# Performance work log

Hardware: AMD Instinct MI355X
Metric: run time of the kernel (lower is better)

## Reference

```python
import jax, jax.numpy as jnp
import numpy as np

H = 16      # attention_head_num
DH = 64     # attention_head_size
D = H * DH  # out_dim = 1024


def setup_inputs() -> dict:
    key = jax.random.key(0)
    ks = jax.random.split(key, 9)
    s = 1.0 / np.sqrt(D)
    x = jax.random.normal(ks[0], (2, 2048, D), dtype=jnp.float32)
    Wq = jax.random.uniform(ks[1], (D, D), jnp.float32, -s, s)
    bq = jax.random.uniform(ks[2], (D,), jnp.float32, -s, s)
    Wk = jax.random.uniform(ks[3], (D, D), jnp.float32, -s, s)
    bk = jax.random.uniform(ks[4], (D,), jnp.float32, -s, s)
    Wv = jax.random.uniform(ks[5], (D, D), jnp.float32, -s, s)
    bv = jax.random.uniform(ks[6], (D,), jnp.float32, -s, s)
    Wo = jax.random.uniform(ks[7], (D, D), jnp.float32, -s, s)
    bo = jax.random.uniform(ks[8], (D,), jnp.float32, -s, s)
    return {"x": x, "Wq": Wq, "bq": bq, "Wk": Wk, "bk": bk,
            "Wv": Wv, "bv": bv, "Wo": Wo, "bo": bo}


def reference(x, Wq, bq, Wk, bk, Wv, bv, Wo, bo):
    B, S, _ = x.shape
    # projections (nn.Linear: x @ W^T + b)
    q = (x @ Wq.T + bq).reshape(B, S, H, DH).transpose(0, 2, 1, 3)  # [B,H,S,Dh]
    k = (x @ Wk.T + bk).reshape(B, S, H, DH).transpose(0, 2, 1, 3)
    v = (x @ Wv.T + bv).reshape(B, S, H, DH).transpose(0, 2, 1, 3)
    scores = jnp.einsum('bhqd,bhkd->bhqk', q, k) / jnp.sqrt(jnp.float32(DH))
    probs = jax.nn.softmax(scores, axis=-1)  # dropout is identity in eval mode
    ctx = jnp.einsum('bhqk,bhkd->bhqd', probs, v)
    ctx = ctx.transpose(0, 2, 1, 3).reshape(B, S, D)
    return ctx @ Wo.T + bo
```

## Files before the change

### kernel.cpp

```cpp
#include <hip/hip_runtime.h>
#include <hip/hip_bf16.h>
#include <stdint.h>

typedef __attribute__((ext_vector_type(8))) short bf16x8;
typedef __attribute__((ext_vector_type(8))) unsigned short u16x8;
typedef __attribute__((ext_vector_type(4))) unsigned short u16x4;
typedef __attribute__((ext_vector_type(4))) float f32x4;

constexpr int NB  = 2;
constexpr int NS  = 2048;
constexpr int NH  = 16;
constexpr int NDH = 64;
constexpr int ND  = 1024;

static __device__ __forceinline__ unsigned short bfbits(float f) {
    union { float f; uint32_t u; } v; v.f = f;
    uint32_t u = v.u + 0x7FFFu + ((v.u >> 16) & 1u);
    return (unsigned short)(u >> 16);
}

static __device__ __forceinline__ float fexp2(float x) {
#if __has_builtin(__builtin_amdgcn_exp2f)
    return __builtin_amdgcn_exp2f(x);
#else
    return exp2f(x);
#endif
}

static __device__ __forceinline__ void gl_lds16(const void* g, void* l) {
    __builtin_amdgcn_global_load_lds(
        (const __attribute__((address_space(1))) unsigned int*)g,
        (__attribute__((address_space(3))) unsigned int*)l, 16, 0, 0);
}

__global__ __launch_bounds__(256)
void cvt_kernel(const float* __restrict__ x,  const float* __restrict__ wq,
                const float* __restrict__ wk, const float* __restrict__ wv,
                const float* __restrict__ wo,
                unsigned short* __restrict__ xb,  unsigned short* __restrict__ wqb,
                unsigned short* __restrict__ wkb, unsigned short* __restrict__ wvb,
                unsigned short* __restrict__ wob)
{
    const int b = blockIdx.x;
    const float* s; unsigned short* d; int off;
    if      (b < 2048) { s = x;  d = xb;  off = b; }
    else if (b < 2560) { s = wq; d = wqb; off = b - 2048; }
    else if (b < 3072) { s = wk; d = wkb; off = b - 2560; }
    else if (b < 3584) { s = wv; d = wvb; off = b - 3072; }
    else               { s = wo; d = wob; off = b - 3584; }
    const size_t idx = ((size_t)off * 256 + threadIdx.x) * 8;
    float4 f0 = *(const float4*)&s[idx];
    float4 f1 = *(const float4*)&s[idx + 4];
    u16x8 o;
    o[0] = bfbits(f0.x); o[1] = bfbits(f0.y); o[2] = bfbits(f0.z); o[3] = bfbits(f0.w);
    o[4] = bfbits(f1.x); o[5] = bfbits(f1.y); o[6] = bfbits(f1.z); o[7] = bfbits(f1.w);
    *(u16x8*)&d[idx] = o;
}

__global__ __launch_bounds__(256, 2)
void qkv_kernel(const unsigned short* __restrict__ xb,
                const unsigned short* __restrict__ wqb,
                const unsigned short* __restrict__ wkb,
                const unsigned short* __restrict__ wvb,
                const float* __restrict__ bq, const float* __restrict__ bk,
                const float* __restrict__ bv,
                unsigned short* __restrict__ qbuf,
                unsigned short* __restrict__ kbuf,
                unsigned short* __restrict__ vtbuf)
{
    __shared__ unsigned short As[128 * 64];
    __shared__ unsigned short Bs[128 * 64];
    __shared__ unsigned short Tt[128][136];

    const int fid = blockIdx.x + blockIdx.y * 24;
    const int xcd = fid & 7, idx = fid >> 3;
    const int bx  = idx >> 2;
    const int by  = xcd * 4 + (idx & 3);

    const int m0  = by * 128;
    const int jg0 = bx * 128;
    const int proj = jg0 >> 10;
    const int n0   = jg0 & 1023;
    const unsigned short* W = (proj == 0) ? wqb : (proj == 1) ? wkb : wvb;
    const float* bias       = (proj == 0) ? bq  : (proj == 1) ? bk  : bv;

    const int tid = threadIdx.x, lane = tid & 63, wid = tid >> 6;
    const int wm = wid >> 1, wn = wid & 1;
    const int l15 = lane & 15, g = lane >> 4;

    const f32x4 fzero = {0.f, 0.f, 0.f, 0.f};
    f32x4 acc[4][4];
#pragma unroll
    for (int i = 0; i < 4; i++)
#pragma unroll
        for (int j = 0; j < 4; j++) acc[i][j] = fzero;

    const int srow = tid >> 3;
    const int scb  = ((tid & 7) * 16) ^ ((srow & 7) << 4);
    const char* asrc = (const char*)xb + (size_t)(m0 + srow) * 2048 + scb;
    const char* bsrc = (const char*)W  + (size_t)(n0 + srow) * 2048 + scb;
    char* adst = (char*)As + tid * 16;
    char* bdst = (char*)Bs + tid * 16;
    const int xm = (l15 & 7) << 4;

    for (int k0 = 0; k0 < 1024; k0 += 64) {
#pragma unroll
        for (int i = 0; i < 4; i++) {
            gl_lds16(asrc + (size_t)i * 32 * 2048 + k0 * 2, adst + i * 4096);
            gl_lds16(bsrc + (size_t)i * 32 * 2048 + k0 * 2, bdst + i * 4096);
        }
        __syncthreads();
#pragma unroll
        for (int kk = 0; kk < 2; kk++) {
            bf16x8 af[4], bfr[4];
#pragma unroll
            for (int i = 0; i < 4; i++) {
                const int row = wm * 64 + i * 16 + l15;
                af[i] = *(const bf16x8*)((const char*)As + row * 128 + ((kk * 64 + g * 16) ^ xm));
            }
#pragma unroll
            for (int j = 0; j < 4; j++) {
                const int row = wn * 64 + j * 16 + l15;
                bfr[j] = *(const bf16x8*)((const char*)Bs + row * 128 + ((kk * 64 + g * 16) ^ xm));
            }
#pragma unroll
            for (int i = 0; i < 4; i++)
#pragma unroll
                for (int j = 0; j < 4; j++)
                    acc[i][j] = __builtin_amdgcn_mfma_f32_16x16x32_bf16(af[i], bfr[j], acc[i][j], 0, 0, 0);
        }
        __syncthreads();
    }

    if (proj < 2) {
        unsigned short* qk_out = (proj == 0) ? qbuf : kbuf;
        const float qs = (proj == 0) ? 0.18033688f : 1.0f;
#pragma unroll
        for (int j = 0; j < 4; j++) {
            const int col = n0 + wn * 64 + j * 16 + l15;
            const float bsv = bias[col];
            const int h = col >> 6, dh = col & 63;
#pragma unroll
            for (int i = 0; i < 4; i++)
#pragma unroll
                for (int r = 0; r < 4; r++) {
                    const int row = m0 + wm * 64 + i * 16 + g * 4 + r;
                    const int b_ = row >> 11, s_ = row & (NS - 1);
                    qk_out[((size_t)((b_ * NH + h) * NS + s_)) * NDH + dh] =
                        bfbits((acc[i][j][r] + bsv) * qs);
                }
        }
    } else {
#pragma unroll
        for (int j = 0; j < 4; j++) {
            const int cl = wn * 64 + j * 16 + l15;
            const float bsv = bias[n0 + cl];
#pragma unroll
            for (int i = 0; i < 4; i++) {
                u16x4 w4;
#pragma unroll
                for (int r = 0; r < 4; r++) w4[r] = bfbits(acc[i][j][r] + bsv);
                *(u16x4*)&Tt[cl][wm * 64 + i * 16 + g * 4] = w4;
            }
        }
        __syncthreads();
        const int b_ = m0 >> 11, s0 = m0 & (NS - 1);
        const int h0 = n0 >> 6;
#pragma unroll
        for (int it = 0; it < 8; it++) {
            const int c = wid * 32 + it * 4 + g;
            u16x8 v8 = *(const u16x8*)&Tt[c][l15 * 8];
            const size_t row = (size_t)(b_ * NH + h0 + (c >> 6)) * NDH + (c & 63);
            *(u16x8*)&vtbuf[row * NS + s0 + l15 * 8] = v8;
        }
    }
}

__global__ __launch_bounds__(512, 4)
void attn_kernel(const unsigned short* __restrict__ qbuf,
                 const unsigned short* __restrict__ kbuf,
                 const unsigned short* __restrict__ vtbuf,
                 unsigned short* __restrict__ ctxbuf)
{
    __shared__ unsigned short Ks[4][64 * 64];
    __shared__ unsigned short Vs[4][64 * 64];

    const int fid  = blockIdx.x + blockIdx.y * 16;
    const int nid  = (fid % 8) * 64 + fid / 8;
    const int bx   = nid % 16, bh = nid / 16;
    const int q0   = bx * 128;

    const int tid = threadIdx.x, lane = tid & 63, wid = tid >> 6;
    const int l15 = lane & 15, g = lane >> 4;

    const unsigned short* qb = qbuf  + (size_t)bh * NS * NDH;
    const unsigned short* kb = kbuf  + (size_t)bh * NS * NDH;
    const unsigned short* vb = vtbuf + (size_t)bh * NDH * NS;

    const int qrow = q0 + wid * 16 + l15;
    const bf16x8 qf0 = *(const bf16x8*)&qb[(size_t)qrow * NDH + g * 8];
    const bf16x8 qf1 = *(const bf16x8*)&qb[(size_t)qrow * NDH + 32 + g * 8];

    const short oneb = (short)0x3F80;
    const bf16x8 ones = {oneb, oneb, oneb, oneb, oneb, oneb, oneb, oneb};

    const f32x4 fzero = {0.f, 0.f, 0.f, 0.f};
    f32x4 acc[4];
#pragma unroll
    for (int d = 0; d < 4; d++) acc[d] = fzero;
    f32x4 acc_l = fzero;

    const int o = tid * 16;
    const int srow = o >> 7;
    const int scb  = (o & 127) ^ ((srow & 7) << 4);
    const char* ksrc = (const char*)kb + srow * 128 + scb;
    const char* vsrc = (const char*)vb + (size_t)srow * (NS * 2) + scb;
    char* kbase = (char*)Ks;
    char* vbase = (char*)Vs;
    const int xm = (l15 & 7) << 4;

    auto STAGE = [&](int b, int t_) {
        gl_lds16(ksrc + (size_t)t_ * 8192, kbase + b * 8192 + o);
        gl_lds16(vsrc + (size_t)t_ * 128,  vbase + b * 8192 + o);
    };

    auto QK = [&](int h, f32x4 (&sv)[4]) {
        const char* ksb = kbase + (h & 3) * 8192;
        __builtin_amdgcn_s_setprio(1);
#pragma unroll
        for (int kt = 0; kt < 4; kt++) {
            const char* rb = ksb + (kt * 16 + l15) * 128;
            bf16x8 kf0 = *(const bf16x8*)(rb + ((g * 16) ^ xm));
            bf16x8 kf1 = *(const bf16x8*)(rb + ((64 + g * 16) ^ xm));
            f32x4 s4 = fzero;
            s4 = __builtin_amdgcn_mfma_f32_16x16x32_bf16(kf0, qf0, s4, 0, 0, 0);
            s4 = __builtin_amdgcn_mfma_f32_16x16x32_bf16(kf1, qf1, s4, 0, 0, 0);
            sv[kt] = s4;
        }
        __builtin_amdgcn_s_setprio(0);
    };

    auto SMPV = [&](int h, f32x4 (&sv)[4]) {
        const char* vsb = vbase + (h & 3) * 8192;
#pragma unroll
        for (int kt = 0; kt < 4; kt++)
#pragma unroll
            for (int r = 0; r < 4; r++)
                sv[kt][r] = fexp2(sv[kt][r]);

        bf16x8 pf[2];
#pragma unroll
        for (int f = 0; f < 2; f++) {
            const int kt0 = f * 2;
            union { __hip_bfloat162 h2; uint32_t u; } c0, c1, c2, c3;
            float2 p01 = { sv[kt0][0], sv[kt0][1] };
            float2 p23 = { sv[kt0][2], sv[kt0][3] };
            float2 p45 = { sv[kt0 + 1][0], sv[kt0 + 1][1] };
            float2 p67 = { sv[kt0 + 1][2], sv[kt0 + 1][3] };
            c0.h2 = __float22bfloat162_rn(p01);
            c1.h2 = __float22bfloat162_rn(p23);
            c2.h2 = __float22bfloat162_rn(p45);
            c3.h2 = __float22bfloat162_rn(p67);
            uint32_t a0 = c0.u, a1 = c1.u, b0 = c2.u, b1 = c3.u;
            asm("v_permlane32_swap_b32 %0, %1" : "+v"(a0), "+v"(b0));
            asm("v_permlane32_swap_b32 %0, %1" : "+v"(a1), "+v"(b1));
            asm("v_permlane16_swap_b32 %0, %1" : "+v"(a0), "+v"(b0));
            asm("v_permlane16_swap_b32 %0, %1" : "+v"(a1), "+v"(b1));
            union { uint32_t w[4]; bf16x8 fr; } r_;
            r_.w[0] = a0; r_.w[1] = a1; r_.w[2] = b0; r_.w[3] = b1;
            pf[f] = r_.fr;
        }

        __builtin_amdgcn_s_setprio(1);
        acc_l = __builtin_amdgcn_mfma_f32_16x16x32_bf16(pf[0], ones, acc_l, 0, 0, 0);
        acc_l = __builtin_amdgcn_mfma_f32_16x16x32_bf16(pf[1], ones, acc_l, 0, 0, 0);
#pragma unroll
        for (int d = 0; d < 4; d++) {
            const char* rb = vsb + (d * 16 + l15) * 128;
            bf16x8 vf0 = *(const bf16x8*)(rb + ((g * 16) ^ xm));
            bf16x8 vf1 = *(const bf16x8*)(rb + ((64 + g * 16) ^ xm));
            acc[d] = __builtin_amdgcn_mfma_f32_16x16x32_bf16(pf[0], vf0, acc[d], 0, 0, 0);
            acc[d] = __builtin_amdgcn_mfma_f32_16x16x32_bf16(pf[1], vf1, acc[d], 0, 0, 0);
        }
        __builtin_amdgcn_s_setprio(0);
    };

    f32x4 svA[4], svB[4];

    STAGE(0, 0); STAGE(1, 1); STAGE(2, 2);
    asm volatile("s_waitcnt vmcnt(4)" ::: "memory");
    __builtin_amdgcn_s_barrier();
    asm volatile("" ::: "memory");
    QK(0, svA);

    for (int t = 0; t < 30; t += 2) {
        asm volatile("s_waitcnt vmcnt(2)" ::: "memory");
        __builtin_amdgcn_s_barrier();
        asm volatile("" ::: "memory");
        STAGE((t + 3) & 3, t + 3);
        QK(t + 1, svB);
        SMPV(t, svA);

        asm volatile("s_waitcnt vmcnt(2)" ::: "memory");
        __builtin_amdgcn_s_barrier();
        asm volatile("" ::: "memory");
        if (t + 4 < 32) STAGE((t + 4) & 3, t + 4);
        QK(t + 2, svA);
        SMPV(t + 1, svB);
    }
    asm volatile("s_waitcnt vmcnt(0)" ::: "memory");
    __builtin_amdgcn_s_barrier();
    asm volatile("" ::: "memory");
    QK(31, svB);
    SMPV(30, svA);
    SMPV(31, svB);

    const int b_ = bh >> 4, h_ = bh & 15;
#pragma unroll
    for (int r = 0; r < 4; r++) {
        const float inv = 1.f / acc_l[r];
        const int sq = q0 + wid * 16 + g * 4 + r;
        const size_t base = ((size_t)(b_ * NS + sq)) * ND + h_ * NDH;
#pragma unroll
        for (int d = 0; d < 4; d++)
            ctxbuf[base + d * 16 + l15] = bfbits(acc[d][r] * inv);
    }
}

__global__ __launch_bounds__(256, 2)
void out_kernel(const unsigned short* __restrict__ ctx,
                const unsigned short* __restrict__ wob,
                const float* __restrict__ bo,
                float* __restrict__ out)
{
    __shared__ unsigned short As[128 * 64];
    __shared__ unsigned short Bs[128 * 64];

    const int n0 = blockIdx.x * 128;
    const int m0 = blockIdx.y * 128;
    const int tid = threadIdx.x, lane = tid & 63, wid = tid >> 6;
    const int wm = wid >> 1, wn = wid & 1;
    const int l15 = lane & 15, g = lane >> 4;

    const f32x4 fzero = {0.f, 0.f, 0.f, 0.f};
    f32x4 acc[4][4];
#pragma unroll
    for (int i = 0; i < 4; i++)
#pragma unroll
        for (int j = 0; j < 4; j++) acc[i][j] = fzero;

    const int srow = tid >> 3;
    const int scb  = ((tid & 7) * 16) ^ ((srow & 7) << 4);
    const char* asrc = (const char*)ctx + (size_t)(m0 + srow) * 2048 + scb;
    const char* bsrc = (const char*)wob + (size_t)(n0 + srow) * 2048 + scb;
    char* adst = (char*)As + tid * 16;
    char* bdst = (char*)Bs + tid * 16;
    const int xm = (l15 & 7) << 4;

    for (int k0 = 0; k0 < 1024; k0 += 64) {
#pragma unroll
        for (int i = 0; i < 4; i++) {
            gl_lds16(asrc + (size_t)i * 32 * 2048 + k0 * 2, adst + i * 4096);
            gl_lds16(bsrc + (size_t)i * 32 * 2048 + k0 * 2, bdst + i * 4096);
        }
        __syncthreads();
#pragma unroll
        for (int kk = 0; kk < 2; kk++) {
            bf16x8 af[4], bfr[4];
#pragma unroll
            for (int i = 0; i < 4; i++) {
                const int row = wm * 64 + i * 16 + l15;
                af[i] = *(const bf16x8*)((const char*)As + row * 128 + ((kk * 64 + g * 16) ^ xm));
            }
#pragma unroll
            for (int j = 0; j < 4; j++) {
                const int row = wn * 64 + j * 16 + l15;
                bfr[j] = *(const bf16x8*)((const char*)Bs + row * 128 + ((kk * 64 + g * 16) ^ xm));
            }
#pragma unroll
            for (int i = 0; i < 4; i++)
#pragma unroll
                for (int j = 0; j < 4; j++)
                    acc[i][j] = __builtin_amdgcn_mfma_f32_16x16x32_bf16(af[i], bfr[j], acc[i][j], 0, 0, 0);
        }
        __syncthreads();
    }

#pragma unroll
    for (int j = 0; j < 4; j++) {
        const int col = n0 + wn * 64 + j * 16 + l15;
        const float bsv = bo[col];
#pragma unroll
        for (int i = 0; i < 4; i++)
#pragma unroll
            for (int r = 0; r < 4; r++) {
                const int row = m0 + wm * 64 + i * 16 + g * 4 + r;
                out[(size_t)row * ND + col] = acc[i][j][r] + bsv;
            }
    }
}

extern "C" void kernel_launch(void* const* d_in, const int* in_sizes, int n_in,
                              void* d_out, int out_size, void* d_ws, size_t ws_size,
                              hipStream_t stream) {
    const float* x  = (const float*)d_in[0];
    const float* Wq = (const float*)d_in[1];
    const float* bq = (const float*)d_in[2];
    const float* Wk = (const float*)d_in[3];
    const float* bk = (const float*)d_in[4];
    const float* Wv = (const float*)d_in[5];
    const float* bv = (const float*)d_in[6];
    const float* Wo = (const float*)d_in[7];
    const float* bo = (const float*)d_in[8];
    float* out = (float*)d_out;

    const size_t qk_elems = (size_t)NB * NH * NS * NDH;
    const size_t w_elems  = (size_t)ND * ND;
    unsigned short* qbuf   = (unsigned short*)d_ws;
    unsigned short* kbuf   = qbuf + qk_elems;
    unsigned short* vtbuf  = kbuf + qk_elems;
    unsigned short* ctxbuf = vtbuf + qk_elems;
    unsigned short* xb     = ctxbuf + qk_elems;
    unsigned short* wqb    = xb + qk_elems;
    unsigned short* wkb    = wqb + w_elems;
    unsigned short* wvb    = wkb + w_elems;
    unsigned short* wob    = wvb + w_elems;

    cvt_kernel<<<4096, 256, 0, stream>>>(x, Wq, Wk, Wv, Wo, xb, wqb, wkb, wvb, wob);
    qkv_kernel<<<dim3(24, 32), 256, 0, stream>>>(xb, wqb, wkb, wvb, bq, bk, bv,
                                                 qbuf, kbuf, vtbuf);
    attn_kernel<<<dim3(16, 32), 512, 0, stream>>>(qbuf, kbuf, vtbuf, ctxbuf);
    out_kernel<<<dim3(8, 32), 256, 0, stream>>>(ctxbuf, wob, bo, out);
}
```

Measured before the change: 115.6 us.

## Process two 16-row query tiles per wave in attention kernel

Each attention wave now handles 32 query rows (two 16-row sub-tiles) instead of 16, so a block covers 256 queries and the grid halves to 8x32 blocks. K and V fragments read from LDS are reused across both sub-tiles, halving global K/V staging traffic and LDS reads per query. The cost is roughly doubled accumulator and score registers, with launch bounds relaxed from 4 to 2 blocks per CU, which lowers occupancy and latency hiding. There are also only 256 blocks, which may underfill the GPU's CUs.

```diff
diff --git a/kernel.cpp b/kernel.cpp
--- a/kernel.cpp
+++ b/kernel.cpp
@@ -176,7 +176,7 @@
     }
 }
 
-__global__ __launch_bounds__(512, 4)
+__global__ __launch_bounds__(512, 2)
 void attn_kernel(const unsigned short* __restrict__ qbuf,
                  const unsigned short* __restrict__ kbuf,
                  const unsigned short* __restrict__ vtbuf,
@@ -185,10 +185,10 @@
     __shared__ unsigned short Ks[4][64 * 64];
     __shared__ unsigned short Vs[4][64 * 64];
 
-    const int fid  = blockIdx.x + blockIdx.y * 16;
-    const int nid  = (fid % 8) * 64 + fid / 8;
-    const int bx   = nid % 16, bh = nid / 16;
-    const int q0   = bx * 128;
+    const int fid  = blockIdx.x + blockIdx.y * 8;
+    const int nid  = (fid & 7) * 32 + (fid >> 3);
+    const int bx   = nid & 7, bh = nid >> 3;
+    const int q0   = bx * 256;
 
     const int tid = threadIdx.x, lane = tid & 63, wid = tid >> 6;
     const int l15 = lane & 15, g = lane >> 4;
@@ -197,18 +197,24 @@
     const unsigned short* kb = kbuf  + (size_t)bh * NS * NDH;
     const unsigned short* vb = vtbuf + (size_t)bh * NDH * NS;
 
-    const int qrow = q0 + wid * 16 + l15;
-    const bf16x8 qf0 = *(const bf16x8*)&qb[(size_t)qrow * NDH + g * 8];
-    const bf16x8 qf1 = *(const bf16x8*)&qb[(size_t)qrow * NDH + 32 + g * 8];
+    bf16x8 qf[2][2];
+#pragma unroll
+    for (int u = 0; u < 2; u++) {
+        const int qrow = q0 + wid * 32 + u * 16 + l15;
+        qf[u][0] = *(const bf16x8*)&qb[(size_t)qrow * NDH + g * 8];
+        qf[u][1] = *(const bf16x8*)&qb[(size_t)qrow * NDH + 32 + g * 8];
+    }
 
     const short oneb = (short)0x3F80;
     const bf16x8 ones = {oneb, oneb, oneb, oneb, oneb, oneb, oneb, oneb};
 
     const f32x4 fzero = {0.f, 0.f, 0.f, 0.f};
-    f32x4 acc[4];
-#pragma unroll
-    for (int d = 0; d < 4; d++) acc[d] = fzero;
-    f32x4 acc_l = fzero;
+    f32x4 acc[2][4];
+#pragma unroll
+    for (int u = 0; u < 2; u++)
+#pragma unroll
+        for (int d = 0; d < 4; d++) acc[u][d] = fzero;
+    f32x4 acc_l[2] = {fzero, fzero};
 
     const int o = tid * 16;
     const int srow = o >> 7;
@@ -224,7 +230,7 @@
         gl_lds16(vsrc + (size_t)t_ * 128,  vbase + b * 8192 + o);
     };
 
-    auto QK = [&](int h, f32x4 (&sv)[4]) {
+    auto QK = [&](int h, f32x4 (&sv)[2][4]) {
         const char* ksb = kbase + (h & 3) * 8192;
         __builtin_amdgcn_s_setprio(1);
 #pragma unroll
@@ -232,60 +238,73 @@
             const char* rb = ksb + (kt * 16 + l15) * 128;
             bf16x8 kf0 = *(const bf16x8*)(rb + ((g * 16) ^ xm));
             bf16x8 kf1 = *(const bf16x8*)(rb + ((64 + g * 16) ^ xm));
-            f32x4 s4 = fzero;
-            s4 = __builtin_amdgcn_mfma_f32_16x16x32_bf16(kf0, qf0, s4, 0, 0, 0);
-            s4 = __builtin_amdgcn_mfma_f32_16x16x32_bf16(kf1, qf1, s4, 0, 0, 0);
-            sv[kt] = s4;
+#pragma unroll
+            for (int u = 0; u < 2; u++) {
+                f32x4 s4 = fzero;
+                s4 = __builtin_amdgcn_mfma_f32_16x16x32_bf16(kf0, qf[u][0], s4, 0, 0, 0);
+                s4 = __builtin_amdgcn_mfma_f32_16x16x32_bf16(kf1, qf[u][1], s4, 0, 0, 0);
+                sv[u][kt] = s4;
+            }
         }
         __builtin_amdgcn_s_setprio(0);
     };
 
-    auto SMPV = [&](int h, f32x4 (&sv)[4]) {
+    auto SMPV = [&](int h, f32x4 (&sv)[2][4]) {
         const char* vsb = vbase + (h & 3) * 8192;
 #pragma unroll
-        for (int kt = 0; kt < 4; kt++)
-#pragma unroll
-            for (int r = 0; r < 4; r++)
-                sv[kt][r] = fexp2(sv[kt][r]);
-
-        bf16x8 pf[2];
-#pragma unroll
-        for (int f = 0; f < 2; f++) {
-            const int kt0 = f * 2;
-            union { __hip_bfloat162 h2; uint32_t u; } c0, c1, c2, c3;
-            float2 p01 = { sv[kt0][0], sv[kt0][1] };
-            float2 p23 = { sv[kt0][2], sv[kt0][3] };
-            float2 p45 = { sv[kt0 + 1][0], sv[kt0 + 1][1] };
-            float2 p67 = { sv[kt0 + 1][2], sv[kt0 + 1][3] };
-            c0.h2 = __float22bfloat162_rn(p01);
-            c1.h2 = __float22bfloat162_rn(p23);
-            c2.h2 = __float22bfloat162_rn(p45);
-            c3.h2 = __float22bfloat162_rn(p67);
-            uint32_t a0 = c0.u, a1 = c1.u, b0 = c2.u, b1 = c3.u;
-            asm("v_permlane32_swap_b32 %0, %1" : "+v"(a0), "+v"(b0));
-            asm("v_permlane32_swap_b32 %0, %1" : "+v"(a1), "+v"(b1));
-            asm("v_permlane16_swap_b32 %0, %1" : "+v"(a0), "+v"(b0));
-            asm("v_permlane16_swap_b32 %0, %1" : "+v"(a1), "+v"(b1));
-            union { uint32_t w[4]; bf16x8 fr; } r_;
-            r_.w[0] = a0; r_.w[1] = a1; r_.w[2] = b0; r_.w[3] = b1;
-            pf[f] = r_.fr;
-        }
+        for (int u = 0; u < 2; u++)
+#pragma unroll
+            for (int kt = 0; kt < 4; kt++)
+#pragma unroll
+                for (int r = 0; r < 4; r++)
+                    sv[u][kt][r] = fexp2(sv[u][kt][r]);
+
+        bf16x8 pf[2][2];
+#pragma unroll
+        for (int u = 0; u < 2; u++)
+#pragma unroll
+            for (int f = 0; f < 2; f++) {
+                const int kt0 = f * 2;
+                union { __hip_bfloat162 h2; uint32_t u32; } c0, c1, c2, c3;
+                float2 p01 = { sv[u][kt0][0], sv[u][kt0][1] };
+                float2 p23 = { sv[u][kt0][2], sv[u][kt0][3] };
+                float2 p45 = { sv[u][kt0 + 1][0], sv[u][kt0 + 1][1] };
+                float2 p67 = { sv[u][kt0 + 1][2], sv[u][kt0 + 1][3] };
+                c0.h2 = __float22bfloat162_rn(p01);
+                c1.h2 = __float22bfloat162_rn(p23);
+                c2.h2 = __float22bfloat162_rn(p45);
+                c3.h2 = __float22bfloat162_rn(p67);
+                uint32_t a0 = c0.u32, a1 = c1.u32, b0 = c2.u32, b1 = c3.u32;
+                asm("v_permlane32_swap_b32 %0, %1" : "+v"(a0), "+v"(b0));
+                asm("v_permlane32_swap_b32 %0, %1" : "+v"(a1), "+v"(b1));
+                asm("v_permlane16_swap_b32 %0, %1" : "+v"(a0), "+v"(b0));
+                asm("v_permlane16_swap_b32 %0, %1" : "+v"(a1), "+v"(b1));
+                union { uint32_t w[4]; bf16x8 fr; } r_;
+                r_.w[0] = a0; r_.w[1] = a1; r_.w[2] = b0; r_.w[3] = b1;
+                pf[u][f] = r_.fr;
+            }
 
         __builtin_amdgcn_s_setprio(1);
-        acc_l = __builtin_amdgcn_mfma_f32_16x16x32_bf16(pf[0], ones, acc_l, 0, 0, 0);
-        acc_l = __builtin_amdgcn_mfma_f32_16x16x32_bf16(pf[1], ones, acc_l, 0, 0, 0);
+#pragma unroll
+        for (int u = 0; u < 2; u++) {
+            acc_l[u] = __builtin_amdgcn_mfma_f32_16x16x32_bf16(pf[u][0], ones, acc_l[u], 0, 0, 0);
+            acc_l[u] = __builtin_amdgcn_mfma_f32_16x16x32_bf16(pf[u][1], ones, acc_l[u], 0, 0, 0);
+        }
 #pragma unroll
         for (int d = 0; d < 4; d++) {
             const char* rb = vsb + (d * 16 + l15) * 128;
             bf16x8 vf0 = *(const bf16x8*)(rb + ((g * 16) ^ xm));
             bf16x8 vf1 = *(const bf16x8*)(rb + ((64 + g * 16) ^ xm));
-            acc[d] = __builtin_amdgcn_mfma_f32_16x16x32_bf16(pf[0], vf0, acc[d], 0, 0, 0);
-            acc[d] = __builtin_amdgcn_mfma_f32_16x16x32_bf16(pf[1], vf1, acc[d], 0, 0, 0);
+#pragma unroll
+            for (int u = 0; u < 2; u++) {
+                acc[u][d] = __builtin_amdgcn_mfma_f32_16x16x32_bf16(pf[u][0], vf0, acc[u][d], 0, 0, 0);
+                acc[u][d] = __builtin_amdgcn_mfma_f32_16x16x32_bf16(pf[u][1], vf1, acc[u][d], 0, 0, 0);
+            }
         }
         __builtin_amdgcn_s_setprio(0);
     };
 
-    f32x4 svA[4], svB[4];
+    f32x4 svA[2][4], svB[2][4];
 
     STAGE(0, 0); STAGE(1, 1); STAGE(2, 2);
     asm volatile("s_waitcnt vmcnt(4)" ::: "memory");
@@ -317,14 +336,16 @@
 
     const int b_ = bh >> 4, h_ = bh & 15;
 #pragma unroll
-    for (int r = 0; r < 4; r++) {
-        const float inv = 1.f / acc_l[r];
-        const int sq = q0 + wid * 16 + g * 4 + r;
-        const size_t base = ((size_t)(b_ * NS + sq)) * ND + h_ * NDH;
-#pragma unroll
-        for (int d = 0; d < 4; d++)
-            ctxbuf[base + d * 16 + l15] = bfbits(acc[d][r] * inv);
-    }
+    for (int u = 0; u < 2; u++)
+#pragma unroll
+        for (int r = 0; r < 4; r++) {
+            const float inv = 1.f / acc_l[u][r];
+            const int sq = q0 + wid * 32 + u * 16 + g * 4 + r;
+            const size_t base = ((size_t)(b_ * NS + sq)) * ND + h_ * NDH;
+#pragma unroll
+            for (int d = 0; d < 4; d++)
+                ctxbuf[base + d * 16 + l15] = bfbits(acc[u][d][r] * inv);
+        }
 }
 
 __global__ __launch_bounds__(256, 2)
@@ -429,6 +450,6 @@
     cvt_kernel<<<4096, 256, 0, stream>>>(x, Wq, Wk, Wv, Wo, xb, wqb, wkb, wvb, wob);
     qkv_kernel<<<dim3(24, 32), 256, 0, stream>>>(xb, wqb, wkb, wvb, bq, bk, bv,
                                                  qbuf, kbuf, vtbuf);
-    attn_kernel<<<dim3(16, 32), 512, 0, stream>>>(qbuf, kbuf, vtbuf, ctxbuf);
+    attn_kernel<<<dim3(8, 32), 512, 0, stream>>>(qbuf, kbuf, vtbuf, ctxbuf);
     out_kernel<<<dim3(8, 32), 256, 0, stream>>>(ctxbuf, wob, bo, out);
 }
```

Measured after the change: 119.2 us. 1.03x slower.
